# Performance work log

Hardware: AMD Instinct MI355X
Metric: run time of the kernel (lower is better)

Reference implementation:

```python
import jax, jax.numpy as jnp
import numpy as np

B, T, D = 4, 2048, 1024
H, DH, E, SEL = 8, 64, 5, 2


def setup_inputs() -> dict:
    key = jax.random.key(0)
    ks = jax.random.split(key, 7)
    s = 0.02
    x = jax.random.normal(ks[0], (B, T, D), dtype=jnp.float32)
    Wq = jax.random.normal(ks[1], (D, H * DH), dtype=jnp.float32) * s
    Wk = jax.random.normal(ks[2], (D, H * DH), dtype=jnp.float32) * s
    Ws = jax.random.normal(ks[3], (D, H * E), dtype=jnp.float32) * s   # gate for V experts
    Wd = jax.random.normal(ks[4], (D, H * E), dtype=jnp.float32) * s   # gate for out experts
    Wv = jax.random.normal(ks[5], (E, D, DH), dtype=jnp.float32) * s   # experts_v weights
    Wo = jax.random.normal(ks[6], (E, DH, D), dtype=jnp.float32) * s   # experts_out weights
    return {"x": x, "Wq": Wq, "Wk": Wk, "Ws": Ws, "Wd": Wd, "Wv": Wv, "Wo": Wo}


def _topk_mask(logits, k):
    # 0/1 mask of top-k experts along last axis (torch.topk indices are distinct)
    _, idx = jax.lax.top_k(logits, k)
    return jnp.sum(jax.nn.one_hot(idx, logits.shape[-1], dtype=logits.dtype), axis=-2)


def reference(x, Wq, Wk, Ws, Wd, Wv, Wo):
    e, d, dh = Wv.shape
    h = Wq.shape[1] // dh
    b, t, _ = x.shape
    scale = dh ** -0.5

    q = (x @ Wq).reshape(b, t, h, dh).transpose(0, 2, 1, 3)  # b h t d
    k = (x @ Wk).reshape(b, t, h, dh).transpose(0, 2, 1, 3)  # b h t d

    # moe_v: per-(b,t,head) top-k experts, sigmoid-weighted combine of expert V projections
    gl_v = (x @ Ws).reshape(b, t, h, e)                      # b t h e
    wv = _topk_mask(gl_v, SEL) * jax.nn.sigmoid(gl_v)        # b t h e (zero off selected)
    xv = jnp.einsum('btd,edk->btek', x, Wv)                  # all-expert V: b t e dh
    v = jnp.einsum('bthe,btek->bhtk', wv, xv)                # b h t dh

    scores = jnp.einsum('bhid,bhjd->bhij', q * scale, k)     # b h t t
    probs = jax.nn.softmax(scores, axis=-1)
    attn = jnp.einsum('bhij,bhjd->bihd', probs, v)           # b t h dh

    # moe_out: top-k selection (weights computed but unused in original), unweighted sum,
    # then sum over heads — fuse both reductions into one einsum
    gl_o = (x @ Wd).reshape(b, t, h, e)
    mask_o = _topk_mask(gl_o, SEL)                           # b t h e
    out = jnp.einsum('bthe,bthk,ekd->btd', mask_o, attn, Wo)  # b t d
    return out
```

## Files before the change

kernel.cpp:

```cpp
#include <hip/hip_runtime.h>
#include <cstdint>
#include <cstddef>

#define BB 4
#define TT 2048
#define DD 1024
#define HH 8
#define DH 64
#define EE 5
#define MM (BB*TT)
#define PLD 1344
#define NWT 1408

typedef short short8 __attribute__((ext_vector_type(8)));
typedef float f32x4  __attribute__((ext_vector_type(4)));

__device__ __forceinline__ float bflo(uint32_t u) { union { uint32_t i; float f; } v; v.i = u << 16; return v.f; }
__device__ __forceinline__ float bfhi(uint32_t u) { union { uint32_t i; float f; } v; v.i = u & 0xFFFF0000u; return v.f; }
__device__ __forceinline__ float bf2f(uint16_t u) { union { uint32_t i; float f; } v; v.i = ((uint32_t)u) << 16; return v.f; }
__device__ __forceinline__ uint32_t pkbf(float a, float b) {
  uint32_t ua = __float_as_uint(a) + 0x8000u;
  uint32_t ub = __float_as_uint(b) + 0x8000u;
  return __builtin_amdgcn_perm(ub, ua, 0x07060302u);
}
__device__ __forceinline__ uint16_t bfr1(float f) {
  return (uint16_t)((__float_as_uint(f) + 0x8000u) >> 16);
}

__device__ __forceinline__ void gload16(const void* g, void* l) {
  __builtin_amdgcn_global_load_lds(
      (const __attribute__((address_space(1))) uint32_t*)g,
      (__attribute__((address_space(3))) uint32_t*)l, 16, 0, 0);
}

__global__ __launch_bounds__(256) void pack_wt_kernel(
    const float* __restrict__ Wq, const float* __restrict__ Wk,
    const float* __restrict__ Wv, uint16_t* __restrict__ Wt)
{
  __shared__ __align__(16) uint16_t Ts[64 * 68];
  int k0 = blockIdx.x * 64, n0 = blockIdx.y * 64;
  int t = threadIdx.x;
#pragma unroll
  for (int rep = 0; rep < 16; ++rep) {
    int li = rep * 256 + t;
    int kl = li >> 6, nl = li & 63;
    int k = k0 + kl, n = n0 + nl;
    float v = 0.f;
    if (n < 512)       v = Wq[k * 512 + n];
    else if (n < 1024) v = Wk[k * 512 + (n - 512)];
    else if (n < 1344) { int nn = n - 1024; v = Wv[((size_t)(nn >> 6) * 1024 + k) * 64 + (nn & 63)]; }
    Ts[kl * 68 + nl] = bfr1(v);
  }
  __syncthreads();
#pragma unroll
  for (int rep = 0; rep < 16; ++rep) {
    int li = rep * 256 + t;
    int nl = li >> 6, kl = li & 63;
    Wt[(size_t)(n0 + nl) * 1024 + k0 + kl] = Ts[kl * 68 + nl];
  }
}

__global__ __launch_bounds__(256) void pack_wot_kernel(
    const float* __restrict__ Wo, uint16_t* __restrict__ WoT)
{
  __shared__ __align__(16) uint16_t Ts[64 * 68];
  int k0 = blockIdx.x * 64, n0 = blockIdx.y * 64;
  int t = threadIdx.x;
#pragma unroll
  for (int rep = 0; rep < 16; ++rep) {
    int li = rep * 256 + t;
    int kl = li >> 6, nl = li & 63;
    Ts[kl * 68 + nl] = bfr1(Wo[(size_t)(k0 + kl) * 1024 + n0 + nl]);
  }
  __syncthreads();
#pragma unroll
  for (int rep = 0; rep < 16; ++rep) {
    int li = rep * 256 + t;
    int nl = li >> 6, kl = li & 63;
    WoT[(size_t)(n0 + nl) * 320 + k0 + kl] = Ts[kl * 68 + nl];
  }
}

__global__ __launch_bounds__(256) void xbf_kernel(const float* __restrict__ x, uint16_t* __restrict__ xb)
{
  int i = (blockIdx.x * 256 + threadIdx.x) * 4;
  float4 v = *(const float4*)(x + i);
  uint2 o;
  o.x = pkbf(v.x, v.y);
  o.y = pkbf(v.z, v.w);
  *(uint2*)(xb + i) = o;
}

__device__ __forceinline__ void top2_5(float g0, float g1, float g2, float g3, float g4,
                                       int& i1, float& b1, int& i2, float& b2) {
  i1 = 0; b1 = g0;
  if (g1 > b1) { b1 = g1; i1 = 1; }
  if (g2 > b1) { b1 = g2; i1 = 2; }
  if (g3 > b1) { b1 = g3; i1 = 3; }
  if (g4 > b1) { b1 = g4; i1 = 4; }
  i2 = -1; b2 = -__builtin_inff();
  if (i1 != 0 && g0 > b2) { b2 = g0; i2 = 0; }
  if (i1 != 1 && g1 > b2) { b2 = g1; i2 = 1; }
  if (i1 != 2 && g2 > b2) { b2 = g2; i2 = 2; }
  if (i1 != 3 && g3 > b2) { b2 = g3; i2 = 3; }
  if (i1 != 4 && g4 > b2) { b2 = g4; i2 = 4; }
}

__device__ __forceinline__ void ldw20(float* d, const float* __restrict__ p) {
#pragma unroll
  for (int j = 0; j < 20; ++j) d[j] = p[j];
}
__device__ __forceinline__ void fma20(float* acc, const float* wv, float xv) {
#pragma unroll
  for (int j = 0; j < 20; ++j) acc[j] = fmaf(xv, wv[j], acc[j]);
}

__global__ __launch_bounds__(1024) void gate_v5_kernel(
    const float* __restrict__ x, const float* __restrict__ Ws,
    const float* __restrict__ Wd, uint32_t* __restrict__ gsel32)
{
  __shared__ __align__(16) float xs[64 * 132];
  int t = threadIdx.x;
  int m0 = blockIdx.x * 64;
  int w = t >> 6, lane = t & 63;
  int cg = __builtin_amdgcn_readfirstlane(w & 3);
  int kq = __builtin_amdgcn_readfirstlane(w >> 2);
  const float* __restrict__ Wg = (cg < 2) ? Ws : Wd;
  const float* __restrict__ wbase = Wg + (size_t)(kq * 32) * 40 + (cg & 1) * 20;

  float acc[20];
#pragma unroll
  for (int j = 0; j < 20; ++j) acc[j] = 0.f;

  for (int tile = 0; tile < 8; ++tile) {
    __syncthreads();
#pragma unroll
    for (int rep = 0; rep < 2; ++rep) {
      int li = rep * 1024 + t;
      int row = li >> 5, kg = li & 31;
      float4 v = *(const float4*)&x[(size_t)(m0 + row) * 1024 + tile * 128 + kg * 4];
      *(float4*)&xs[row * 132 + kg * 4] = v;
    }
    __syncthreads();

    const float* wp = wbase + (size_t)tile * 128 * 40;
    const float* xp = &xs[lane * 132 + kq * 32];
    float wc[20], wn[20];
    ldw20(wc, wp);
#pragma unroll
    for (int k4 = 0; k4 < 8; ++k4) {
      float4 xv = *(const float4*)&xp[k4 * 4];
      ldw20(wn, wp + (size_t)(k4 * 4 + 1) * 40);
      fma20(acc, wc, xv.x);
      ldw20(wc, wp + (size_t)(k4 * 4 + 2) * 40);
      fma20(acc, wn, xv.y);
      ldw20(wn, wp + (size_t)(k4 * 4 + 3) * 40);
      fma20(acc, wc, xv.z);
      if (k4 < 7) ldw20(wc, wp + (size_t)(k4 * 4 + 4) * 40);
      fma20(acc, wn, xv.w);
    }
  }

  float* red = xs;
  int ro = cg * (64 * 21) + lane * 21;
  __syncthreads();
  if (kq == 1) {
#pragma unroll
    for (int j = 0; j < 20; ++j) red[ro + j] = acc[j];
  }
  __syncthreads();
  if (kq == 0) {
#pragma unroll
    for (int j = 0; j < 20; ++j) acc[j] += red[ro + j];
  }
  __syncthreads();
  if (kq == 3) {
#pragma unroll
    for (int j = 0; j < 20; ++j) red[ro + j] = acc[j];
  }
  __syncthreads();
  if (kq == 2) {
#pragma unroll
    for (int j = 0; j < 20; ++j) acc[j] += red[ro + j];
  }
  __syncthreads();
  if (kq == 2) {
#pragma unroll
    for (int j = 0; j < 20; ++j) red[ro + j] = acc[j];
  }
  __syncthreads();

  if (kq == 0) {
#pragma unroll
    for (int j = 0; j < 20; ++j) acc[j] += red[ro + j];
    int m = m0 + lane;
    if (cg < 2) {
#pragma unroll
      for (int hh = 0; hh < 4; ++hh) {
        int i1, i2; float b1, b2;
        top2_5(acc[hh * 5 + 0], acc[hh * 5 + 1], acc[hh * 5 + 2],
               acc[hh * 5 + 3], acc[hh * 5 + 4], i1, b1, i2, b2);
        float w1 = 1.f / (1.f + __expf(-b1));
        float w2 = 1.f / (1.f + __expf(-b2));
        uint32_t* g = gsel32 + ((size_t)m * 8 + (cg & 1) * 4 + hh) * 4;
        g[0] = __float_as_uint(w1);
        g[1] = __float_as_uint(w2);
        g[2] = (uint32_t)(i1 | (i2 << 3));
      }
    } else {
#pragma unroll
      for (int hh = 0; hh < 4; ++hh) {
        int j1, j2; float c1, c2;
        top2_5(acc[hh * 5 + 0], acc[hh * 5 + 1], acc[hh * 5 + 2],
               acc[hh * 5 + 3], acc[hh * 5 + 4], j1, c1, j2, c2);
        uint32_t* g = gsel32 + ((size_t)m * 8 + (cg & 1) * 4 + hh) * 4;
        g[3] = (uint32_t)(j1 | (j2 << 3));
      }
    }
  }
}

__global__ __launch_bounds__(256) void proj_mfma_kernel(
    const uint16_t* __restrict__ xb, const uint16_t* __restrict__ Wt,
    uint16_t* __restrict__ proj)
{
  __shared__ __align__(16) uint16_t As[128 * 32];
  __shared__ __align__(16) uint16_t Bs[128 * 32];
  int t = threadIdx.x;
  int n0 = blockIdx.x * 128, m0 = blockIdx.y * 128;
  int w = t >> 6, lane = t & 63, q = lane >> 4, c = lane & 15;
  int wm = w & 1, wn = w >> 1;
  int lr = lane >> 2, lc = (lane & 3) * 8;
  f32x4 zf = {0.f, 0.f, 0.f, 0.f};
  f32x4 acc[4][4];
#pragma unroll
  for (int i = 0; i < 4; ++i)
#pragma unroll
    for (int j = 0; j < 4; ++j) acc[i][j] = zf;

  for (int kb = 0; kb < 32; ++kb) {
    __syncthreads();
#pragma unroll
    for (int j = 0; j < 2; ++j) {
      int row = w * 32 + j * 16 + lr;
      gload16(xb + (size_t)(m0 + row) * 1024 + kb * 32 + lc,
              &As[(w * 32 + j * 16) * 32 + lane * 8]);
      gload16(Wt + (size_t)(n0 + row) * 1024 + kb * 32 + lc,
              &Bs[(w * 32 + j * 16) * 32 + lane * 8]);
    }
    __syncthreads();
    short8 af[4], bfr[4];
#pragma unroll
    for (int i = 0; i < 4; ++i)
      af[i] = *(const short8*)&As[(wm * 64 + i * 16 + c) * 32 + q * 8];
#pragma unroll
    for (int j = 0; j < 4; ++j)
      bfr[j] = *(const short8*)&Bs[(wn * 64 + j * 16 + c) * 32 + q * 8];
#pragma unroll
    for (int i = 0; i < 4; ++i)
#pragma unroll
      for (int j = 0; j < 4; ++j)
        acc[i][j] = __builtin_amdgcn_mfma_f32_16x16x32_bf16(af[i], bfr[j], acc[i][j], 0, 0, 0);
  }
#pragma unroll
  for (int i = 0; i < 4; ++i)
#pragma unroll
    for (int j = 0; j < 4; ++j) {
      int col = n0 + wn * 64 + j * 16 + c;
      if (col < PLD) {
#pragma unroll
        for (int reg = 0; reg < 4; ++reg) {
          int row = m0 + wm * 64 + i * 16 + q * 4 + reg;
          proj[(size_t)row * PLD + col] = bfr1(acc[i][j][reg]);
        }
      }
    }
}

__global__ __launch_bounds__(256) void out_mfma_kernel(
    const uint16_t* __restrict__ zb, const uint16_t* __restrict__ WoT,
    float* __restrict__ out)
{
  __shared__ __align__(16) uint16_t As[128 * 32];
  __shared__ __align__(16) uint16_t Bs[128 * 32];
  int t = threadIdx.x;
  int n0 = blockIdx.x * 128, m0 = blockIdx.y * 128;
  int w = t >> 6, lane = t & 63, q = lane >> 4, c = lane & 15;
  int wm = w & 1, wn = w >> 1;
  int lr = lane >> 2, lc = (lane & 3) * 8;
  f32x4 zf = {0.f, 0.f, 0.f, 0.f};
  f32x4 acc[4][4];
#pragma unroll
  for (int i = 0; i < 4; ++i)
#pragma unroll
    for (int j = 0; j < 4; ++j) acc[i][j] = zf;

  for (int kb = 0; kb < 10; ++kb) {
    __syncthreads();
#pragma unroll
    for (int j = 0; j < 2; ++j) {
      int row = w * 32 + j * 16 + lr;
      gload16(zb + (size_t)(m0 + row) * 320 + kb * 32 + lc,
              &As[(w * 32 + j * 16) * 32 + lane * 8]);
      gload16(WoT + (size_t)(n0 + row) * 320 + kb * 32 + lc,
              &Bs[(w * 32 + j * 16) * 32 + lane * 8]);
    }
    __syncthreads();
    short8 af[4], bfr[4];
#pragma unroll
    for (int i = 0; i < 4; ++i)
      af[i] = *(const short8*)&As[(wm * 64 + i * 16 + c) * 32 + q * 8];
#pragma unroll
    for (int j = 0; j < 4; ++j)
      bfr[j] = *(const short8*)&Bs[(wn * 64 + j * 16 + c) * 32 + q * 8];
#pragma unroll
    for (int i = 0; i < 4; ++i)
#pragma unroll
      for (int j = 0; j < 4; ++j)
        acc[i][j] = __builtin_amdgcn_mfma_f32_16x16x32_bf16(af[i], bfr[j], acc[i][j], 0, 0, 0);
  }
#pragma unroll
  for (int i = 0; i < 4; ++i)
#pragma unroll
    for (int j = 0; j < 4; ++j) {
      int col = n0 + wn * 64 + j * 16 + c;
#pragma unroll
      for (int reg = 0; reg < 4; ++reg) {
        int row = m0 + wm * 64 + i * 16 + q * 4 + reg;
        out[(size_t)row * 1024 + col] = acc[i][j][reg];
      }
    }
}

__global__ __launch_bounds__(256) void vbuild_kernel(
    const uint16_t* __restrict__ proj, const uint4* __restrict__ gsel,
    uint16_t* __restrict__ vt)
{
  int bi = blockIdx.x;
  int bh = bi >> 5, tb = bi & 31;
  int b = bh >> 3, h = bh & 7;
  int t = threadIdx.x;
  int tt = t & 63, dg = t >> 6;
  int m = b * 2048 + tb * 64 + tt;
  uint4 gs = gsel[m * 8 + h];
  float w1 = __uint_as_float(gs.x), w2 = __uint_as_float(gs.y);
  int i1 = gs.z & 7, i2 = (gs.z >> 3) & 7;
  const uint16_t* base = proj + (size_t)m * PLD + 1024;
  const uint4* p1 = (const uint4*)(base + i1 * 64 + dg * 16);
  const uint4* p2 = (const uint4*)(base + i2 * 64 + dg * 16);
  uint4 A0 = p1[0], A1 = p1[1], B0 = p2[0], B1 = p2[1];
  float v[16];
  v[0]  = w1*bflo(A0.x) + w2*bflo(B0.x); v[1]  = w1*bfhi(A0.x) + w2*bfhi(B0.x);
  v[2]  = w1*bflo(A0.y) + w2*bflo(B0.y); v[3]  = w1*bfhi(A0.y) + w2*bfhi(B0.y);
  v[4]  = w1*bflo(A0.z) + w2*bflo(B0.z); v[5]  = w1*bfhi(A0.z) + w2*bfhi(B0.z);
  v[6]  = w1*bflo(A0.w) + w2*bflo(B0.w); v[7]  = w1*bfhi(A0.w) + w2*bfhi(B0.w);
  v[8]  = w1*bflo(A1.x) + w2*bflo(B1.x); v[9]  = w1*bfhi(A1.x) + w2*bfhi(B1.x);
  v[10] = w1*bflo(A1.y) + w2*bflo(B1.y); v[11] = w1*bfhi(A1.y) + w2*bfhi(B1.y);
  v[12] = w1*bflo(A1.z) + w2*bflo(B1.z); v[13] = w1*bfhi(A1.z) + w2*bfhi(B1.z);
  v[14] = w1*bflo(A1.w) + w2*bflo(B1.w); v[15] = w1*bfhi(A1.w) + w2*bfhi(B1.w);
  int pcol = ((tt & 15) << 2) | (tt >> 4);
#pragma unroll
  for (int dd = 0; dd < 16; ++dd)
    vt[(size_t)(bh * 64 + dg * 16 + dd) * 2048 + tb * 64 + pcol] = bfr1(v[dd]);
}

__global__ __launch_bounds__(256, 4) void flash_mfma_kernel(
    const uint16_t* __restrict__ proj, const uint16_t* __restrict__ vt,
    uint16_t* __restrict__ attnb)
{
  __shared__ __align__(16) uint16_t Ks[64 * 72];
  __shared__ __align__(16) uint16_t Vs[64 * 72];
  __shared__ __align__(16) uint16_t Ps[64 * 72];
  int t = threadIdx.x;
  int bx = blockIdx.x;
  int qb = bx & 31, bh = bx >> 5;
  int h = bh & 7, b = bh >> 3;
  int w = t >> 6, lane = t & 63, q = lane >> 4, c = lane & 15;
  int srow = t >> 2, scq = t & 3;

  short8 aq[2];
  {
    const uint16_t* qp = proj + (size_t)(b * 2048 + qb * 64 + w * 16 + c) * PLD + h * 64;
    aq[0] = *(const short8*)(qp + q * 8);
    aq[1] = *(const short8*)(qp + 32 + q * 8);
  }

  f32x4 zf = {0.f, 0.f, 0.f, 0.f};
  f32x4 of[4];
  float ls[4];
#pragma unroll
  for (int nt = 0; nt < 4; ++nt) { of[nt] = zf; ls[nt] = 0.f; }

  const uint16_t* kg = proj + (size_t)(b * 2048 + srow) * PLD + 512 + h * 64 + scq * 16;
  const uint16_t* vg = vt + (size_t)(bh * 64 + srow) * 2048 + scq * 16;
  uint4 kp0, kp1, vp0, vp1;
  kp0 = ((const uint4*)kg)[0]; kp1 = ((const uint4*)kg)[1];
  vp0 = ((const uint4*)vg)[0]; vp1 = ((const uint4*)vg)[1];

  for (int it = 0; it < 32; ++it) {
    if (it) __syncthreads();
    *(uint4*)&Ks[srow * 72 + scq * 16] = kp0;
    *(uint4*)&Ks[srow * 72 + scq * 16 + 8] = kp1;
    *(uint4*)&Vs[srow * 72 + scq * 16] = vp0;
    *(uint4*)&Vs[srow * 72 + scq * 16 + 8] = vp1;
    __syncthreads();
    if (it < 31) {
      const uint4* pk = (const uint4*)(kg + (size_t)(it + 1) * 64 * PLD);
      kp0 = pk[0]; kp1 = pk[1];
      const uint4* pv = (const uint4*)(vg + (it + 1) * 64);
      vp0 = pv[0]; vp1 = pv[1];
    }

    short8 bk[4][2];
#pragma unroll
    for (int nt = 0; nt < 4; ++nt) {
      bk[nt][0] = *(const short8*)&Ks[(nt * 16 + c) * 72 + q * 8];
      bk[nt][1] = *(const short8*)&Ks[(nt * 16 + c) * 72 + 32 + q * 8];
    }
    f32x4 sf[4];
#pragma unroll
    for (int nt = 0; nt < 4; ++nt) {
      f32x4 s = __builtin_amdgcn_mfma_f32_16x16x32_bf16(aq[0], bk[nt][0], zf, 0, 0, 0);
      sf[nt] = __builtin_amdgcn_mfma_f32_16x16x32_bf16(aq[1], bk[nt][1], s, 0, 0, 0);
    }

#pragma unroll
    for (int reg = 0; reg < 4; ++reg) {
      float p0 = __builtin_amdgcn_exp2f(sf[0][reg] * 0.18033688f);
      float p1 = __builtin_amdgcn_exp2f(sf[1][reg] * 0.18033688f);
      float p2 = __builtin_amdgcn_exp2f(sf[2][reg] * 0.18033688f);
      float p3 = __builtin_amdgcn_exp2f(sf[3][reg] * 0.18033688f);
      ls[reg] += (p0 + p1) + (p2 + p3);
      uint2 pw;
      pw.x = pkbf(p0, p1);
      pw.y = pkbf(p2, p3);
      *(uint2*)&Ps[(w * 16 + q * 4 + reg) * 72 + c * 4] = pw;
    }

    short8 bv[4][2];
#pragma unroll
    for (int nt = 0; nt < 4; ++nt) {
      bv[nt][0] = *(const short8*)&Vs[(nt * 16 + c) * 72 + q * 8];
      bv[nt][1] = *(const short8*)&Vs[(nt * 16 + c) * 72 + 32 + q * 8];
    }
    short8 ap0 = *(const short8*)&Ps[(w * 16 + c) * 72 + q * 8];
    short8 ap1 = *(const short8*)&Ps[(w * 16 + c) * 72 + 32 + q * 8];
#pragma unroll
    for (int nt = 0; nt < 4; ++nt) {
      of[nt] = __builtin_amdgcn_mfma_f32_16x16x32_bf16(ap0, bv[nt][0], of[nt], 0, 0, 0);
      of[nt] = __builtin_amdgcn_mfma_f32_16x16x32_bf16(ap1, bv[nt][1], of[nt], 0, 0, 0);
    }
  }

#pragma unroll
  for (int reg = 0; reg < 4; ++reg) {
    float s = ls[reg];
    s += __shfl_xor(s, 1);
    s += __shfl_xor(s, 2);
    s += __shfl_xor(s, 4);
    s += __shfl_xor(s, 8);
    float inv = 1.0f / s;
    size_t row = (size_t)(b * 2048 + qb * 64 + w * 16 + q * 4 + reg);
#pragma unroll
    for (int nt = 0; nt < 4; ++nt)
      attnb[row * 512 + h * 64 + nt * 16 + c] = bfr1(of[nt][reg] * inv);
  }
}

__global__ __launch_bounds__(64) void zbuild_kernel(
    const uint16_t* __restrict__ attnb, const uint32_t* __restrict__ gselw,
    uint16_t* __restrict__ zbuf)
{
  int m = blockIdx.x; int c = threadIdx.x;
  float acc[5] = {0.f, 0.f, 0.f, 0.f, 0.f};
#pragma unroll
  for (int h = 0; h < 8; ++h) {
    uint32_t sel = gselw[(m * 8 + h) * 4 + 3];
    int e1 = sel & 7, e2 = (sel >> 3) & 7;
    float a = bf2f(attnb[(size_t)m * 512 + h * 64 + c]);
#pragma unroll
    for (int e = 0; e < 5; ++e)
      acc[e] += (e == e1 || e == e2) ? a : 0.f;
  }
#pragma unroll
  for (int e = 0; e < 5; ++e)
    zbuf[(size_t)m * 320 + e * 64 + c] = bfr1(acc[e]);
}

extern "C" void kernel_launch(void* const* d_in, const int* in_sizes, int n_in,
                              void* d_out, int out_size, void* d_ws, size_t ws_size,
                              hipStream_t stream) {
  const float* x  = (const float*)d_in[0];
  const float* Wq = (const float*)d_in[1];
  const float* Wk = (const float*)d_in[2];
  const float* Ws = (const float*)d_in[3];
  const float* Wd = (const float*)d_in[4];
  const float* Wv = (const float*)d_in[5];
  const float* Wo = (const float*)d_in[6];
  float* out = (float*)d_out;

  char* ws = (char*)d_ws;
  uint4*    gsel  = (uint4*)   (ws);
  uint16_t* WoT   = (uint16_t*)(ws + 1048576);
  uint16_t* Wt    = (uint16_t*)(ws + 1703936);
  uint16_t* xb    = (uint16_t*)(ws + 4587520);
  uint16_t* proj  = (uint16_t*)(ws + 21364736);
  uint16_t* vt    = (uint16_t*)(ws + 43384832);
  uint16_t* attnb = (uint16_t*)(ws + 1703936);
  uint16_t* zbuf  = (uint16_t*)(ws + 10092544);

  gate_v5_kernel<<<MM / 64, 1024, 0, stream>>>(x, Ws, Wd, (uint32_t*)gsel);
  pack_wt_kernel<<<dim3(16, 22), 256, 0, stream>>>(Wq, Wk, Wv, Wt);
  pack_wot_kernel<<<dim3(5, 16), 256, 0, stream>>>(Wo, WoT);
  xbf_kernel<<<(MM * DD / 4) / 256, 256, 0, stream>>>(x, xb);
  proj_mfma_kernel<<<dim3(NWT / 128, MM / 128), 256, 0, stream>>>(xb, Wt, proj);
  vbuild_kernel<<<32 * 32, 256, 0, stream>>>(proj, gsel, vt);
  flash_mfma_kernel<<<BB * HH * (TT / 64), 256, 0, stream>>>(proj, vt, attnb);
  zbuild_kernel<<<MM, 64, 0, stream>>>(attnb, (const uint32_t*)gsel, zbuf);
  out_mfma_kernel<<<dim3(DD / 128, MM / 128), 256, 0, stream>>>(zbuf, WoT, out);
}
```

Baseline: 273.1 us.

## Rewrite flash attention with 32x32 MFMA and register-resident P via permlane swap

The attention kernel now uses 32x32x16 bf16 MFMA with 128 query rows per block, computing S transposed (K as A operand) so the probabilities can be repacked in registers with v_cvt_pk_bf16_f32 and permlane32_swap instead of going through an LDS P buffer. This removes the P shared-memory round trip and halves K/V tile reloads per query row. The V-build kernel drops its column permutation to match the new operand layout. It adds register pressure, since the occupancy hint is removed, and halves the grid size, which risks lower occupancy.

```diff
diff --git a/kernel.cpp b/kernel.cpp
--- a/kernel.cpp
+++ b/kernel.cpp
@@ -14,6 +14,8 @@
 
 typedef short short8 __attribute__((ext_vector_type(8)));
 typedef float f32x4  __attribute__((ext_vector_type(4)));
+typedef float f32x16 __attribute__((ext_vector_type(16)));
+typedef unsigned int u32x2 __attribute__((ext_vector_type(2)));
 
 __device__ __forceinline__ float bflo(uint32_t u) { union { uint32_t i; float f; } v; v.i = u << 16; return v.f; }
 __device__ __forceinline__ float bfhi(uint32_t u) { union { uint32_t i; float f; } v; v.i = u & 0xFFFF0000u; return v.f; }
@@ -25,6 +27,11 @@
 }
 __device__ __forceinline__ uint16_t bfr1(float f) {
   return (uint16_t)((__float_as_uint(f) + 0x8000u) >> 16);
+}
+__device__ __forceinline__ uint32_t cvtpk(float a, float b) {
+  uint32_t r;
+  asm("v_cvt_pk_bf16_f32 %0, %1, %2" : "=v"(r) : "v"(a), "v"(b));
+  return r;
 }
 
 __device__ __forceinline__ void gload16(const void* g, void* l) {
@@ -358,38 +365,37 @@
   v[10] = w1*bflo(A1.y) + w2*bflo(B1.y); v[11] = w1*bfhi(A1.y) + w2*bfhi(B1.y);
   v[12] = w1*bflo(A1.z) + w2*bflo(B1.z); v[13] = w1*bfhi(A1.z) + w2*bfhi(B1.z);
   v[14] = w1*bflo(A1.w) + w2*bflo(B1.w); v[15] = w1*bfhi(A1.w) + w2*bfhi(B1.w);
-  int pcol = ((tt & 15) << 2) | (tt >> 4);
 #pragma unroll
   for (int dd = 0; dd < 16; ++dd)
-    vt[(size_t)(bh * 64 + dg * 16 + dd) * 2048 + tb * 64 + pcol] = bfr1(v[dd]);
-}
-
-__global__ __launch_bounds__(256, 4) void flash_mfma_kernel(
+    vt[(size_t)(bh * 64 + dg * 16 + dd) * 2048 + tb * 64 + tt] = bfr1(v[dd]);
+}
+
+__global__ __launch_bounds__(256) void flash_mfma_kernel(
     const uint16_t* __restrict__ proj, const uint16_t* __restrict__ vt,
     uint16_t* __restrict__ attnb)
 {
   __shared__ __align__(16) uint16_t Ks[64 * 72];
   __shared__ __align__(16) uint16_t Vs[64 * 72];
-  __shared__ __align__(16) uint16_t Ps[64 * 72];
+  __shared__ float lsb[4 * 32];
   int t = threadIdx.x;
   int bx = blockIdx.x;
-  int qb = bx & 31, bh = bx >> 5;
+  int qb = bx & 15, bh = bx >> 4;
   int h = bh & 7, b = bh >> 3;
-  int w = t >> 6, lane = t & 63, q = lane >> 4, c = lane & 15;
+  int w = t >> 6, lane = t & 63;
+  int r31 = lane & 31, hi = lane >> 5;
   int srow = t >> 2, scq = t & 3;
 
-  short8 aq[2];
+  short8 qf[4];
   {
-    const uint16_t* qp = proj + (size_t)(b * 2048 + qb * 64 + w * 16 + c) * PLD + h * 64;
-    aq[0] = *(const short8*)(qp + q * 8);
-    aq[1] = *(const short8*)(qp + 32 + q * 8);
-  }
-
-  f32x4 zf = {0.f, 0.f, 0.f, 0.f};
-  f32x4 of[4];
-  float ls[4];
-#pragma unroll
-  for (int nt = 0; nt < 4; ++nt) { of[nt] = zf; ls[nt] = 0.f; }
+    const uint16_t* qp = proj + (size_t)(b * 2048 + qb * 128 + w * 32 + r31) * PLD + h * 64 + hi * 8;
+#pragma unroll
+    for (int f = 0; f < 4; ++f) qf[f] = *(const short8*)(qp + 16 * f);
+  }
+
+  f32x16 o0 = {0.f}, o1 = {0.f};
+#pragma unroll
+  for (int i = 0; i < 16; ++i) { o0[i] = 0.f; o1[i] = 0.f; }
+  float lsacc = 0.f;
 
   const uint16_t* kg = proj + (size_t)(b * 2048 + srow) * PLD + 512 + h * 64 + scq * 16;
   const uint16_t* vg = vt + (size_t)(bh * 64 + srow) * 2048 + scq * 16;
@@ -411,59 +417,55 @@
       vp0 = pv[0]; vp1 = pv[1];
     }
 
-    short8 bk[4][2];
-#pragma unroll
-    for (int nt = 0; nt < 4; ++nt) {
-      bk[nt][0] = *(const short8*)&Ks[(nt * 16 + c) * 72 + q * 8];
-      bk[nt][1] = *(const short8*)&Ks[(nt * 16 + c) * 72 + 32 + q * 8];
-    }
-    f32x4 sf[4];
-#pragma unroll
-    for (int nt = 0; nt < 4; ++nt) {
-      f32x4 s = __builtin_amdgcn_mfma_f32_16x16x32_bf16(aq[0], bk[nt][0], zf, 0, 0, 0);
-      sf[nt] = __builtin_amdgcn_mfma_f32_16x16x32_bf16(aq[1], bk[nt][1], s, 0, 0, 0);
-    }
-
-#pragma unroll
-    for (int reg = 0; reg < 4; ++reg) {
-      float p0 = __builtin_amdgcn_exp2f(sf[0][reg] * 0.18033688f);
-      float p1 = __builtin_amdgcn_exp2f(sf[1][reg] * 0.18033688f);
-      float p2 = __builtin_amdgcn_exp2f(sf[2][reg] * 0.18033688f);
-      float p3 = __builtin_amdgcn_exp2f(sf[3][reg] * 0.18033688f);
-      ls[reg] += (p0 + p1) + (p2 + p3);
-      uint2 pw;
-      pw.x = pkbf(p0, p1);
-      pw.y = pkbf(p2, p3);
-      *(uint2*)&Ps[(w * 16 + q * 4 + reg) * 72 + c * 4] = pw;
-    }
-
-    short8 bv[4][2];
-#pragma unroll
-    for (int nt = 0; nt < 4; ++nt) {
-      bv[nt][0] = *(const short8*)&Vs[(nt * 16 + c) * 72 + q * 8];
-      bv[nt][1] = *(const short8*)&Vs[(nt * 16 + c) * 72 + 32 + q * 8];
-    }
-    short8 ap0 = *(const short8*)&Ps[(w * 16 + c) * 72 + q * 8];
-    short8 ap1 = *(const short8*)&Ps[(w * 16 + c) * 72 + 32 + q * 8];
-#pragma unroll
-    for (int nt = 0; nt < 4; ++nt) {
-      of[nt] = __builtin_amdgcn_mfma_f32_16x16x32_bf16(ap0, bv[nt][0], of[nt], 0, 0, 0);
-      of[nt] = __builtin_amdgcn_mfma_f32_16x16x32_bf16(ap1, bv[nt][1], of[nt], 0, 0, 0);
-    }
-  }
-
-#pragma unroll
-  for (int reg = 0; reg < 4; ++reg) {
-    float s = ls[reg];
-    s += __shfl_xor(s, 1);
-    s += __shfl_xor(s, 2);
-    s += __shfl_xor(s, 4);
-    s += __shfl_xor(s, 8);
-    float inv = 1.0f / s;
-    size_t row = (size_t)(b * 2048 + qb * 64 + w * 16 + q * 4 + reg);
-#pragma unroll
-    for (int nt = 0; nt < 4; ++nt)
-      attnb[row * 512 + h * 64 + nt * 16 + c] = bfr1(of[nt][reg] * inv);
+    short8 pa[4];
+#pragma unroll
+    for (int jg = 0; jg < 2; ++jg) {
+      f32x16 s;
+#pragma unroll
+      for (int i = 0; i < 16; ++i) s[i] = 0.f;
+#pragma unroll
+      for (int f = 0; f < 4; ++f) {
+        short8 kf = *(const short8*)&Ks[(jg * 32 + r31) * 72 + hi * 8 + 16 * f];
+        s = __builtin_amdgcn_mfma_f32_32x32x16_bf16(kf, qf[f], s, 0, 0, 0);
+      }
+      float p[16];
+#pragma unroll
+      for (int reg = 0; reg < 16; ++reg)
+        p[reg] = __builtin_amdgcn_exp2f(s[reg] * 0.18033688f);
+      lsacc += (((p[0] + p[1]) + (p[2] + p[3])) + ((p[4] + p[5]) + (p[6] + p[7])))
+             + (((p[8] + p[9]) + (p[10] + p[11])) + ((p[12] + p[13]) + (p[14] + p[15])));
+      uint32_t X1 = cvtpk(p[0], p[1]),  X2 = cvtpk(p[2], p[3]);
+      uint32_t Y1 = cvtpk(p[4], p[5]),  Y2 = cvtpk(p[6], p[7]);
+      uint32_t Z1 = cvtpk(p[8], p[9]),  Z2 = cvtpk(p[10], p[11]);
+      uint32_t W1 = cvtpk(p[12], p[13]), W2 = cvtpk(p[14], p[15]);
+      u32x2 s1 = __builtin_amdgcn_permlane32_swap(X1, Y1, false, false);
+      u32x2 s2 = __builtin_amdgcn_permlane32_swap(X2, Y2, false, false);
+      u32x2 s3 = __builtin_amdgcn_permlane32_swap(Z1, W1, false, false);
+      u32x2 s4 = __builtin_amdgcn_permlane32_swap(Z2, W2, false, false);
+      uint4 f0 = { s1.x, s2.x, s1.y, s2.y };
+      uint4 f1 = { s3.x, s4.x, s3.y, s4.y };
+      pa[jg * 2 + 0] = *(short8*)&f0;
+      pa[jg * 2 + 1] = *(short8*)&f1;
+    }
+
+#pragma unroll
+    for (int f = 0; f < 4; ++f) {
+      short8 vf0 = *(const short8*)&Vs[(r31) * 72 + hi * 8 + 16 * f];
+      short8 vf1 = *(const short8*)&Vs[(32 + r31) * 72 + hi * 8 + 16 * f];
+      o0 = __builtin_amdgcn_mfma_f32_32x32x16_bf16(pa[f], vf0, o0, 0, 0, 0);
+      o1 = __builtin_amdgcn_mfma_f32_32x32x16_bf16(pa[f], vf1, o1, 0, 0, 0);
+    }
+  }
+
+  float lsc = lsacc + __shfl_xor(lsacc, 32);
+  if (lane < 32) lsb[w * 32 + r31] = 1.0f / lsc;
+#pragma unroll
+  for (int reg = 0; reg < 16; ++reg) {
+    int r = (reg & 3) + 8 * (reg >> 2) + 4 * hi;
+    float inv = lsb[w * 32 + r];
+    size_t row = (size_t)(b * 2048 + qb * 128 + w * 32 + r);
+    attnb[row * 512 + h * 64 + r31]      = bfr1(o0[reg] * inv);
+    attnb[row * 512 + h * 64 + 32 + r31] = bfr1(o1[reg] * inv);
   }
 }
 
@@ -515,7 +517,7 @@
   xbf_kernel<<<(MM * DD / 4) / 256, 256, 0, stream>>>(x, xb);
   proj_mfma_kernel<<<dim3(NWT / 128, MM / 128), 256, 0, stream>>>(xb, Wt, proj);
   vbuild_kernel<<<32 * 32, 256, 0, stream>>>(proj, gsel, vt);
-  flash_mfma_kernel<<<BB * HH * (TT / 64), 256, 0, stream>>>(proj, vt, attnb);
+  flash_mfma_kernel<<<BB * HH * (TT / 128), 256, 0, stream>>>(proj, vt, attnb);
   zbuild_kernel<<<MM, 64, 0, stream>>>(attnb, (const uint32_t*)gsel, zbuf);
   out_mfma_kernel<<<dim3(DD / 128, MM / 128), 256, 0, stream>>>(zbuf, WoT, out);
 }
```

Result: faster. 253.8 us (-7.1%).
